# Performance work log

Measured on AMD Instinct MI355X. Metric: run time of the kernel, lower is better.

The kernel has to match this reference:

```python
import jax, jax.numpy as jnp
import numpy as np

N = 4096
D = 256
DEG = 32
E0 = N * DEG
RATIO = 0.5
NEG_SLOPE = 0.2


def setup_inputs() -> dict:
    key = jax.random.key(0)
    ks = jax.random.split(key, 12)
    # edges with NO self loops (so appending all N self-loops == add_remaining_self_loops)
    src = jax.random.randint(ks[0], (E0,), 0, N, dtype=jnp.int32)
    off = jax.random.randint(ks[1], (E0,), 1, N, dtype=jnp.int32)
    dst = ((src + off) % N).astype(jnp.int32)
    edge_index = jnp.stack([src, dst])
    edge_weight = jnp.ones((E0,), jnp.float32)
    x = jax.random.normal(ks[2], (N, D), jnp.float32)
    s = 1.0 / np.sqrt(D)
    u = lambda k, shp: jax.random.uniform(k, shp, jnp.float32, -s, s)
    return {
        'x': x,
        'edge_index': edge_index,
        'edge_weight': edge_weight,
        'lin_w': u(ks[3], (D, D)), 'lin_b': u(ks[4], (D,)),
        'att_w': jax.random.uniform(ks[5], (2 * D, 1), jnp.float32, -1.0 / np.sqrt(2 * D), 1.0 / np.sqrt(2 * D)),
        'att_b': u(ks[6], (1,)),
        'le1_w': u(ks[7], (D, 1)), 'le1_b': u(ks[8], (1,)),
        'le2_w': u(ks[9], (D, 1)),
        'le3_w': u(ks[10], (D, 1)), 'le3_b': u(ks[11], (1,)),
    }


def reference(x, edge_index, edge_weight, lin_w, lin_b, att_w, att_b,
              le1_w, le1_b, le2_w, le3_w, le3_b):
    n, d = x.shape
    # add_remaining_self_loops (input has no self loops by construction)
    loop = jnp.arange(n, dtype=edge_index.dtype)
    src = jnp.concatenate([edge_index[0], loop])
    dst = jnp.concatenate([edge_index[1], loop])
    w = jnp.concatenate([edge_weight, jnp.ones((n,), edge_weight.dtype)])

    # GNN is None -> x_pool = x
    x_pool_j = x[src]                                        # [E, D] gather
    x_q = jax.ops.segment_max(x_pool_j, dst, num_segments=n)  # scatter-max
    x_q_e = (x_q @ lin_w + lin_b)[dst]                        # [E, D]
    # att(cat([x_q, x_pool_j])) without materializing [E, 2D]
    score = x_q_e @ att_w[:d, 0] + x_pool_j @ att_w[d:, 0] + att_b[0]
    score = jax.nn.leaky_relu(score, NEG_SLOPE)
    # segment softmax over destination nodes
    smax = jax.ops.segment_max(score, dst, num_segments=n)
    ex = jnp.exp(score - smax[dst])
    denom = jax.ops.segment_sum(ex, dst, num_segments=n)
    score = ex / denom[dst]
    # dropout p=0 -> no-op
    xn = jax.ops.segment_sum(x_pool_j * score[:, None], dst, num_segments=n)

    # LEConv fitness: sigmoid( lin3(x) + sum_j (lin1(x_j) - lin2(x_i)) )
    a = xn @ le1_w + le1_b          # [N, 1]
    b = xn @ le2_w                  # [N, 1] (no bias)
    agg = jax.ops.segment_sum(a[src] - b[dst], dst, num_segments=n)
    fitness = jax.nn.sigmoid((agg + xn @ le3_w + le3_b)[:, 0])

    k = int(np.ceil(RATIO * N))
    _, perm = jax.lax.top_k(fitness, k)
    x_out = xn[perm] * fitness[perm][:, None]

    # Coarsening A_c = S[:, perm]^T @ A @ S[:, perm]; dense since SpGEMM nnz is data-dependent
    S = jnp.zeros((n, n), x.dtype).at[src, dst].add(score)[:, perm]  # [N, k]
    A = jnp.zeros((n, n), x.dtype).at[src, dst].add(w)               # [N, N]
    A_c = S.T @ (A @ S)                                              # [k, k]
    A_c = A_c * (1.0 - jnp.eye(k, dtype=A_c.dtype))                  # remove_diag
    return x_out, A_c, perm
```

## Files before the change

kernel.cpp:

```cpp
#include <hip/hip_runtime.h>
#include <cstdint>
#include <cstddef>
#include <math.h>

#define NN   4096
#define DD   256
#define E0S  131072
#define NE   (E0S + NN)
#define KK   2048
#define NEG_SLOPE 0.2f
#define SEGCAP 256

typedef float floatx4 __attribute__((ext_vector_type(4)));

__device__ __forceinline__ int esrc(const int* s, int e){ return e < E0S ? s[e] : e - E0S; }
__device__ __forceinline__ int edst(const int* d, int e){ return e < E0S ? d[e] : e - E0S; }

__global__ void init_kernel(int* deg_dst, int* deg_src, int* colmap, float* Ac, int zero_ac){
    int i = blockIdx.x * blockDim.x + threadIdx.x;
    int stride = gridDim.x * blockDim.x;
    if (zero_ac){
        for (size_t t = i; t < (size_t)KK * KK; t += stride) Ac[t] = 0.f;
    }
    for (int t = i; t < NN; t += stride){ deg_dst[t] = 0; deg_src[t] = 0; colmap[t] = -1; }
}

__global__ void count_kernel(const int* e_src, const int* e_dst, int* deg_dst, int* deg_src){
    int e = blockIdx.x * blockDim.x + threadIdx.x;
    if (e < NE){
        atomicAdd(&deg_dst[edst(e_dst, e)], 1);
        atomicAdd(&deg_src[esrc(e_src, e)], 1);
    }
}

__global__ void __launch_bounds__(1024) scan_kernel(const int* degA, int* offA, int* curA,
                                                    const int* degB, int* offB, int* curB){
    const int* deg = (blockIdx.x == 0) ? degA : degB;
    int* off = (blockIdx.x == 0) ? offA : offB;
    int* cur = (blockIdx.x == 0) ? curA : curB;
    __shared__ int part[1024];
    int t = threadIdx.x;
    int base = t * 4;
    int s0 = deg[base], s1 = deg[base+1], s2 = deg[base+2], s3 = deg[base+3];
    int tot = s0 + s1 + s2 + s3;
    part[t] = tot;
    __syncthreads();
    for (int d = 1; d < 1024; d <<= 1){
        int v = (t >= d) ? part[t - d] : 0;
        __syncthreads();
        part[t] += v;
        __syncthreads();
    }
    int excl = part[t] - tot;
    off[base]   = excl;            cur[base]   = excl;
    off[base+1] = excl + s0;       cur[base+1] = excl + s0;
    off[base+2] = excl + s0 + s1;  cur[base+2] = excl + s0 + s1;
    off[base+3] = excl + s0 + s1 + s2; cur[base+3] = excl + s0 + s1 + s2;
    if (t == 1023) off[NN] = part[1023];
}

__global__ void fill_kernel(const int* e_src, const int* e_dst, int* cur_dst, int* cur_src,
                            int* eid_dst, int* eid_src){
    int e = blockIdx.x * blockDim.x + threadIdx.x;
    if (e < NE){
        int p = atomicAdd(&cur_dst[edst(e_dst, e)], 1); eid_dst[p] = e;
        int q = atomicAdd(&cur_src[esrc(e_src, e)], 1); eid_src[q] = e;
    }
}

__global__ void segsort_kernel(const int* off_dst, int* eid_dst, const int* off_src, int* eid_src,
                               const int* e_src, int* isd){
    __shared__ int buf[4][SEGCAP];
    int wid  = (blockIdx.x * blockDim.x + threadIdx.x) >> 6;
    int lane = threadIdx.x & 63;
    int w    = threadIdx.x >> 6;
    const int* off; int* eid; int n; bool isdst;
    if (wid < NN){ off = off_dst; eid = eid_dst; n = wid; isdst = true; }
    else         { off = off_src; eid = eid_src; n = wid - NN; isdst = false; }
    int lo = off[n], hi = off[n+1];
    int L = hi - lo;
    int Lc = (L <= SEGCAP) ? L : SEGCAP;
    for (int i = lane; i < Lc; i += 64) buf[w][i] = eid[lo + i];
    __syncthreads();
    if (L <= SEGCAP){
        for (int i = lane; i < L; i += 64){
            int v = buf[w][i];
            int r = 0;
            for (int j = 0; j < L; ++j) r += (buf[w][j] < v);
            eid[lo + r] = v;
            if (isdst) isd[lo + r] = esrc(e_src, v);
        }
    } else if (lane == 0){
        for (int i = lo + 1; i < hi; ++i){
            int v = eid[i]; int j = i - 1;
            while (j >= lo && eid[j] > v){ eid[j+1] = eid[j]; --j; }
            eid[j+1] = v;
        }
        if (isdst) for (int i = lo; i < hi; ++i) isd[i] = esrc(e_src, eid[i]);
    }
}

__global__ void segmax_kernel(const float* x, const int* off, const int* isd, float* x_q){
    __shared__ int is_[4][SEGCAP];
    int g = threadIdx.x >> 6;
    int l = threadIdx.x & 63;
    int n = blockIdx.x * 4 + g;
    int lo = off[n], hi = off[n+1];
    int L = hi - lo;
    int Ls = (L <= SEGCAP) ? L : SEGCAP;
    for (int t = l; t < Ls; t += 64) is_[g][t] = isd[lo + t];
    __syncthreads();
    int c0 = l * 4;
    floatx4 m = {-INFINITY, -INFINITY, -INFINITY, -INFINITY};
    int t = 0;
    for (; t + 1 < Ls; t += 2){
        floatx4 v0 = *(const floatx4*)&x[(size_t)is_[g][t]   * DD + c0];
        floatx4 v1 = *(const floatx4*)&x[(size_t)is_[g][t+1] * DD + c0];
        m.x = fmaxf(m.x, fmaxf(v0.x, v1.x));
        m.y = fmaxf(m.y, fmaxf(v0.y, v1.y));
        m.z = fmaxf(m.z, fmaxf(v0.z, v1.z));
        m.w = fmaxf(m.w, fmaxf(v0.w, v1.w));
    }
    if (t < Ls){
        floatx4 v0 = *(const floatx4*)&x[(size_t)is_[g][t] * DD + c0];
        m.x = fmaxf(m.x, v0.x); m.y = fmaxf(m.y, v0.y);
        m.z = fmaxf(m.z, v0.z); m.w = fmaxf(m.w, v0.w);
    }
    for (t = Ls; t < L; ++t){
        floatx4 v0 = *(const floatx4*)&x[(size_t)isd[lo + t] * DD + c0];
        m.x = fmaxf(m.x, v0.x); m.y = fmaxf(m.y, v0.y);
        m.z = fmaxf(m.z, v0.z); m.w = fmaxf(m.w, v0.w);
    }
    *(floatx4*)&x_q[(size_t)n * DD + c0] = m;
}

#define LR2 4
__global__ void linnd_kernel(const float* x, const float* x_q,
                             const float* lin_w, const float* lin_b, const float* att_w,
                             float* q_s, float* p_s){
    __shared__ float xs[LR2][DD];
    __shared__ float s1[256], s2[256];
    int col = threadIdx.x;
    int r0 = blockIdx.x * LR2;
    for (int r = 0; r < LR2; ++r) xs[r][col] = x_q[(size_t)(r0 + r) * DD + col];
    __syncthreads();
    float acc[LR2];
    float bc = lin_b[col];
    #pragma unroll
    for (int r = 0; r < LR2; ++r) acc[r] = bc;
    for (int kk = 0; kk < DD; ++kk){
        float wv = lin_w[(size_t)kk * DD + col];
        #pragma unroll
        for (int r = 0; r < LR2; ++r) acc[r] = fmaf(xs[r][kk], wv, acc[r]);
    }
    float aw1 = att_w[col];
    float aw2 = att_w[DD + col];
    for (int r = 0; r < LR2; ++r){
        int n = r0 + r;
        s1[col] = acc[r] * aw1;
        s2[col] = x[(size_t)n * DD + col] * aw2;
        __syncthreads();
        for (int d = 128; d > 0; d >>= 1){
            if (col < d){ s1[col] += s1[col + d]; s2[col] += s2[col + d]; }
            __syncthreads();
        }
        if (col == 0){ q_s[n] = s1[0]; p_s[n] = s2[0]; }
        __syncthreads();
    }
}

__global__ void softxn_kernel(const float* x, const int* off, const int* eid, const int* isd,
                              const float* q_s, const float* p_s, const float* att_b,
                              const float* le1_w, const float* le1_b, const float* le2_w,
                              const float* le3_w, const float* le3_b,
                              float* sc, float* ssd, float* xn,
                              float* a_, float* b_, float* c_){
    __shared__ int   is_[SEGCAP];
    __shared__ float ss_[SEGCAP];
    __shared__ float s1[256], s2[256], s3[256];
    int n = blockIdx.x, col = threadIdx.x;
    int lo = off[n], hi = off[n+1];
    int L = hi - lo;
    int Ls = (L <= SEGCAP) ? L : SEGCAP;
    for (int t = col; t < Ls; t += 256) is_[t] = isd[lo + t];
    __syncthreads();
    if (col < 64){
        int lane = col;
        float ab = att_b[0];
        float qn = q_s[n];
        float m = -INFINITY;
        for (int t = lane; t < L; t += 64){
            int sn = (t < Ls) ? is_[t] : isd[lo + t];
            float s = qn + p_s[sn] + ab;
            s = (s > 0.f) ? s : NEG_SLOPE * s;
            m = fmaxf(m, s);
        }
        #pragma unroll
        for (int d = 32; d > 0; d >>= 1) m = fmaxf(m, __shfl_xor(m, d));
        float sum = 0.f;
        for (int t = lane; t < L; t += 64){
            int sn = (t < Ls) ? is_[t] : isd[lo + t];
            float s = qn + p_s[sn] + ab;
            s = (s > 0.f) ? s : NEG_SLOPE * s;
            float ex = expf(s - m);
            if (t < Ls) ss_[t] = ex; else ssd[lo + t] = ex;
            sum += ex;
        }
        #pragma unroll
        for (int d = 32; d > 0; d >>= 1) sum += __shfl_xor(sum, d);
        float inv = 1.f / sum;
        for (int t = lane; t < L; t += 64){
            float v = ((t < Ls) ? ss_[t] : ssd[lo + t]) * inv;
            if (t < Ls) ss_[t] = v;
            ssd[lo + t] = v;
            sc[eid[lo + t]] = v;
        }
    }
    __syncthreads();
    float acc = 0.f;
    int t = 0;
    for (; t + 1 < Ls; t += 2){
        float v0 = x[(size_t)is_[t]   * DD + col];
        float v1 = x[(size_t)is_[t+1] * DD + col];
        acc = fmaf(ss_[t],   v0, acc);
        acc = fmaf(ss_[t+1], v1, acc);
    }
    if (t < Ls) acc = fmaf(ss_[t], x[(size_t)is_[t] * DD + col], acc);
    for (t = Ls; t < L; ++t)
        acc = fmaf(ssd[lo + t], x[(size_t)isd[lo + t] * DD + col], acc);
    xn[(size_t)n * DD + col] = acc;
    s1[col] = acc * le1_w[col];
    s2[col] = acc * le2_w[col];
    s3[col] = acc * le3_w[col];
    __syncthreads();
    for (int dd = 128; dd > 0; dd >>= 1){
        if (col < dd){ s1[col] += s1[col+dd]; s2[col] += s2[col+dd]; s3[col] += s3[col+dd]; }
        __syncthreads();
    }
    if (col == 0){
        a_[n] = s1[0] + le1_b[0];
        b_[n] = s2[0];
        c_[n] = s3[0] + le3_b[0];
    }
}

__global__ void fitness_kernel(const int* off, const int* isd,
                               const float* a_, const float* b_, const float* c_,
                               float* fit){
    int wave = threadIdx.x >> 6;
    int lane = threadIdx.x & 63;
    int n = blockIdx.x * 4 + wave;
    int lo = off[n], hi = off[n+1];
    float bn = b_[n];
    float s = 0.f;
    for (int t = lo + lane; t < hi; t += 64){
        s += a_[isd[t]] - bn;
    }
    #pragma unroll
    for (int d = 32; d > 0; d >>= 1) s += __shfl_xor(s, d);
    if (lane == 0){
        float z = s + c_[n];
        fit[n] = 1.f / (1.f + expf(-z));
    }
}

__global__ void __launch_bounds__(1024) topk_kernel(const float* fit, int* perm, int* colmap,
                                                    float* out_perm){
    __shared__ unsigned long long keys[NN];
    int t = threadIdx.x;
    for (int i = t; i < NN; i += 1024){
        unsigned int u = __float_as_uint(fit[i]);
        u = (u & 0x80000000u) ? ~u : (u | 0x80000000u);
        u = ~u;
        keys[i] = ((unsigned long long)u << 32) | (unsigned int)i;
    }
    __syncthreads();
    for (unsigned int ssize = 2; ssize <= NN; ssize <<= 1){
        for (unsigned int stride = ssize >> 1; stride > 0; stride >>= 1){
            for (int i = t; i < NN / 2; i += 1024){
                unsigned int idx = 2u * i - (i & (stride - 1u));
                unsigned int par = idx + stride;
                bool asc = ((idx & ssize) == 0u);
                unsigned long long a = keys[idx], b = keys[par];
                if ((a > b) == asc){ keys[idx] = b; keys[par] = a; }
            }
            __syncthreads();
        }
    }
    for (int i = t; i < KK; i += 1024){
        int node = (int)(keys[i] & 0xFFFFFFFFull);
        perm[i] = node;
        colmap[node] = i;
        out_perm[i] = (float)node;
    }
}

__global__ void xoutprep_kernel(const float* xn, const float* fit, const int* perm, float* x_out,
                                const int* eid_src, const int* e_dst, const int* colmap,
                                const float* sc, int* cp, float* sp){
    int b = blockIdx.x;
    if (b < KK){
        int r = b, d = threadIdx.x;
        int p = perm[r];
        x_out[(size_t)r * DD + d] = xn[(size_t)p * DD + d] * fit[p];
    } else {
        int u = (b - KK) * 256 + threadIdx.x;
        if (u < NE){
            int f = eid_src[u];
            cp[u] = colmap[edst(e_dst, f)];
            sp[u] = sc[f];
        }
    }
}

__global__ void spgemm1_kernel(const int* e_dst, const float* ew,
                               const int* off_src, const int* eid_src,
                               const int* cp, const float* sp, float* T){
    __shared__ float row[KK];
    __shared__ int   jlo_[SEGCAP];
    __shared__ int   jhi_[SEGCAP];
    __shared__ float w_[SEGCAP];
    int i = blockIdx.x;
    for (int c = threadIdx.x; c < KK; c += 256) row[c] = 0.f;
    int lo = off_src[i], hi = off_src[i+1];
    int L = hi - lo;
    int Ls = (L <= SEGCAP) ? L : SEGCAP;
    for (int t = threadIdx.x; t < Ls; t += 256){
        int e = eid_src[lo + t];
        int j = edst(e_dst, e);
        jlo_[t] = off_src[j];
        jhi_[t] = off_src[j+1];
        w_[t]   = (e < E0S) ? ew[e] : 1.0f;
    }
    __syncthreads();
    int sw = threadIdx.x >> 5, ln = threadIdx.x & 31;
    for (int t = sw; t < Ls; t += 8){
        float w1 = w_[t];
        for (int u = jlo_[t] + ln; u < jhi_[t]; u += 32){
            int c = cp[u];
            if (c >= 0) atomicAdd(&row[c], w1 * sp[u]);
        }
    }
    for (int t = Ls + sw; t < L; t += 8){
        int e = eid_src[lo + t];
        int j = edst(e_dst, e);
        float w1 = (e < E0S) ? ew[e] : 1.0f;
        int jlo = off_src[j], jhi = off_src[j+1];
        for (int u = jlo + ln; u < jhi; u += 32){
            int c = cp[u];
            if (c >= 0) atomicAdd(&row[c], w1 * sp[u]);
        }
    }
    __syncthreads();
    float* Trow = T + (size_t)i * KK;
    for (int c = threadIdx.x; c < KK; c += 256) Trow[c] = row[c];
}

__global__ void spgemm2_kernel(const int* perm, const int* off_dst,
                               const int* isd, const float* ssd,
                               const float* T, float* Ac){
    __shared__ int   is_[8][SEGCAP];
    __shared__ float ss_[8][SEGCAP];
    int bx = blockIdx.x;
    int by = blockIdx.y;
    int half = by >> 8;
    int rr   = by & 255;
    int sub  = threadIdx.x >> 5;
    int lane = threadIdx.x & 31;
    int r = rr * 8 + sub;
    int chunk = bx + 8 * half;
    int c0 = chunk * 128 + lane * 4;
    int node = perm[r];
    int lo = off_dst[node], hi = off_dst[node+1];
    int L = hi - lo;
    int Ls = (L <= SEGCAP) ? L : SEGCAP;
    for (int t = lane; t < Ls; t += 32){
        is_[sub][t] = isd[lo + t];
        ss_[sub][t] = ssd[lo + t];
    }
    __syncthreads();
    floatx4 acc = {0.f, 0.f, 0.f, 0.f};
    int t = 0;
    for (; t + 1 < Ls; t += 2){
        floatx4 a = *(const floatx4*)&T[(size_t)is_[sub][t]   * KK + c0];
        floatx4 b = *(const floatx4*)&T[(size_t)is_[sub][t+1] * KK + c0];
        float s0 = ss_[sub][t], s1 = ss_[sub][t+1];
        acc.x = fmaf(s0, a.x, acc.x); acc.y = fmaf(s0, a.y, acc.y);
        acc.z = fmaf(s0, a.z, acc.z); acc.w = fmaf(s0, a.w, acc.w);
        acc.x = fmaf(s1, b.x, acc.x); acc.y = fmaf(s1, b.y, acc.y);
        acc.z = fmaf(s1, b.z, acc.z); acc.w = fmaf(s1, b.w, acc.w);
    }
    for (; t < Ls; ++t){
        floatx4 a = *(const floatx4*)&T[(size_t)is_[sub][t] * KK + c0];
        float s0 = ss_[sub][t];
        acc.x = fmaf(s0, a.x, acc.x); acc.y = fmaf(s0, a.y, acc.y);
        acc.z = fmaf(s0, a.z, acc.z); acc.w = fmaf(s0, a.w, acc.w);
    }
    for (t = Ls; t < L; ++t){
        floatx4 a = *(const floatx4*)&T[(size_t)isd[lo + t] * KK + c0];
        float s0 = ssd[lo + t];
        acc.x = fmaf(s0, a.x, acc.x); acc.y = fmaf(s0, a.y, acc.y);
        acc.z = fmaf(s0, a.z, acc.z); acc.w = fmaf(s0, a.w, acc.w);
    }
    if (r - c0 >= 0 && r - c0 < 4){
        if (r - c0 == 0) acc.x = 0.f;
        else if (r - c0 == 1) acc.y = 0.f;
        else if (r - c0 == 2) acc.z = 0.f;
        else acc.w = 0.f;
    }
    __builtin_nontemporal_store(acc, (floatx4*)&Ac[(size_t)r * KK + c0]);
}

__global__ void ac_kernel(const int* e_src, const int* e_dst, const float* ew,
                          const int* off_src,
                          const int* cp, const float* sp, float* Ac){
    int e1 = blockIdx.x * blockDim.x + threadIdx.x;
    if (e1 >= NE) return;
    int i = (e1 < E0S) ? e_src[e1] : e1 - E0S;
    int j = (e1 < E0S) ? e_dst[e1] : e1 - E0S;
    float w1 = (e1 < E0S) ? ew[e1] : 1.0f;
    int ilo = off_src[i], ihi = off_src[i+1];
    int jlo = off_src[j], jhi = off_src[j+1];
    for (int ta = ilo; ta < ihi; ++ta){
        int ca = cp[ta];
        if (ca < 0) continue;
        float va = sp[ta] * w1;
        float* rowp = Ac + (size_t)ca * KK;
        for (int tb = jlo; tb < jhi; ++tb){
            int cb = cp[tb];
            if (cb < 0) continue;
            atomicAdd(&rowp[cb], va * sp[tb]);
        }
    }
}

__global__ void diag_kernel(float* Ac){
    int r = blockIdx.x * blockDim.x + threadIdx.x;
    if (r < KK) Ac[(size_t)r * KK + r] = 0.f;
}

extern "C" void kernel_launch(void* const* d_in, const int* in_sizes, int n_in,
                              void* d_out, int out_size, void* d_ws, size_t ws_size,
                              hipStream_t stream){
    const float* x     = (const float*)d_in[0];
    const int*   ei    = (const int*)d_in[1];
    const float* ew    = (const float*)d_in[2];
    const float* lin_w = (const float*)d_in[3];
    const float* lin_b = (const float*)d_in[4];
    const float* att_w = (const float*)d_in[5];
    const float* att_b = (const float*)d_in[6];
    const float* le1_w = (const float*)d_in[7];
    const float* le1_b = (const float*)d_in[8];
    const float* le2_w = (const float*)d_in[9];
    const float* le3_w = (const float*)d_in[10];
    const float* le3_b = (const float*)d_in[11];

    const int* e_src = ei;
    const int* e_dst = ei + E0S;

    float* out    = (float*)d_out;
    float* x_out  = out;
    float* Ac     = out + (size_t)KK * DD;
    float* operm  = out + (size_t)KK * DD + (size_t)KK * KK;

    char* wp = (char*)d_ws;
    auto alloc_i = [&](size_t n){ int* p = (int*)wp; wp += n * sizeof(int); return p; };
    auto alloc_f = [&](size_t n){ float* p = (float*)wp; wp += n * sizeof(float); return p; };

    int* deg_dst = alloc_i(NN);
    int* deg_src = alloc_i(NN);
    int* off_dst = alloc_i(NN + 1);
    int* off_src = alloc_i(NN + 1);
    int* cur_dst = alloc_i(NN);
    int* cur_src = alloc_i(NN);
    int* eid_dst = alloc_i(NE);
    int* eid_src = alloc_i(NE);
    int* colmap  = alloc_i(NN);
    int* perm    = alloc_i(KK);
    int* isd     = alloc_i(NE);
    int* cp      = alloc_i(NE);
    float* sp    = alloc_f(NE);
    float* ssd   = alloc_f(NE);
    float* q_s   = alloc_f(NN);
    float* p_s   = alloc_f(NN);
    float* a_    = alloc_f(NN);
    float* b_    = alloc_f(NN);
    float* c_    = alloc_f(NN);
    float* fit   = alloc_f(NN);
    float* sc    = alloc_f(NE);
    float* x_q   = alloc_f((size_t)NN * DD);
    float* xn    = alloc_f((size_t)NN * DD);
    float* T     = alloc_f((size_t)NN * KK);
    bool dense_ok = ((size_t)(wp - (char*)d_ws) <= ws_size);
    (void)n_in; (void)in_sizes; (void)out_size;

    const int EB = (NE + 255) / 256;

    init_kernel<<<2048, 256, 0, stream>>>(deg_dst, deg_src, colmap, Ac, dense_ok ? 0 : 1);
    count_kernel<<<EB, 256, 0, stream>>>(e_src, e_dst, deg_dst, deg_src);
    scan_kernel<<<2, 1024, 0, stream>>>(deg_dst, off_dst, cur_dst, deg_src, off_src, cur_src);
    fill_kernel<<<EB, 256, 0, stream>>>(e_src, e_dst, cur_dst, cur_src, eid_dst, eid_src);
    segsort_kernel<<<(2 * NN) / 4, 256, 0, stream>>>(off_dst, eid_dst, off_src, eid_src, e_src, isd);
    segmax_kernel<<<NN / 4, 256, 0, stream>>>(x, off_dst, isd, x_q);
    linnd_kernel<<<NN / LR2, 256, 0, stream>>>(x, x_q, lin_w, lin_b, att_w, q_s, p_s);
    softxn_kernel<<<NN, 256, 0, stream>>>(x, off_dst, eid_dst, isd, q_s, p_s, att_b,
                                          le1_w, le1_b, le2_w, le3_w, le3_b,
                                          sc, ssd, xn, a_, b_, c_);
    fitness_kernel<<<NN / 4, 256, 0, stream>>>(off_dst, isd, a_, b_, c_, fit);
    topk_kernel<<<1, 1024, 0, stream>>>(fit, perm, colmap, operm);
    xoutprep_kernel<<<KK + EB, 256, 0, stream>>>(xn, fit, perm, x_out,
                                                 eid_src, e_dst, colmap, sc, cp, sp);
    if (dense_ok){
        spgemm1_kernel<<<NN, 256, 0, stream>>>(e_dst, ew, off_src, eid_src, cp, sp, T);
        spgemm2_kernel<<<dim3(8, 512), 256, 0, stream>>>(perm, off_dst, isd, ssd, T, Ac);
    } else {
        ac_kernel<<<EB, 256, 0, stream>>>(e_src, e_dst, ew, off_src, cp, sp, Ac);
        diag_kernel<<<(KK + 255) / 256, 256, 0, stream>>>(Ac);
    }
}
```

Before: 212.7 us.

## Process four nodes per block in softxn with float4 gathers and wave reductions

The softmax/aggregation kernel now assigns one 64-lane wave per destination node, with four nodes per block, instead of one 256-thread block per node. Each lane gathers four contiguous features with float4 loads, and the LEConv dot products use wave shuffles instead of a shared-memory tree reduction with repeated block barriers. Previously three of four waves sat idle during the softmax phase, and the reduction needed many __syncthreads; now every wave does useful work throughout. The init kernel also launches far fewer blocks when the Ac zeroing is not needed.

Result: faster. 204.5 us (-3.8%).

```diff
diff --git a/kernel.cpp b/kernel.cpp
--- a/kernel.cpp
+++ b/kernel.cpp
@@ -175,22 +175,22 @@
                               const float* le3_w, const float* le3_b,
                               float* sc, float* ssd, float* xn,
                               float* a_, float* b_, float* c_){
-    __shared__ int   is_[SEGCAP];
-    __shared__ float ss_[SEGCAP];
-    __shared__ float s1[256], s2[256], s3[256];
-    int n = blockIdx.x, col = threadIdx.x;
+    __shared__ int   is_[4][SEGCAP];
+    __shared__ float ss_[4][SEGCAP];
+    int g = threadIdx.x >> 6;
+    int l = threadIdx.x & 63;
+    int n = blockIdx.x * 4 + g;
     int lo = off[n], hi = off[n+1];
     int L = hi - lo;
     int Ls = (L <= SEGCAP) ? L : SEGCAP;
-    for (int t = col; t < Ls; t += 256) is_[t] = isd[lo + t];
-    __syncthreads();
-    if (col < 64){
-        int lane = col;
+    for (int t = l; t < Ls; t += 64) is_[g][t] = isd[lo + t];
+    __syncthreads();
+    {
         float ab = att_b[0];
         float qn = q_s[n];
         float m = -INFINITY;
-        for (int t = lane; t < L; t += 64){
-            int sn = (t < Ls) ? is_[t] : isd[lo + t];
+        for (int t = l; t < L; t += 64){
+            int sn = (t < Ls) ? is_[g][t] : isd[lo + t];
             float s = qn + p_s[sn] + ab;
             s = (s > 0.f) ? s : NEG_SLOPE * s;
             m = fmaxf(m, s);
@@ -198,49 +198,72 @@
         #pragma unroll
         for (int d = 32; d > 0; d >>= 1) m = fmaxf(m, __shfl_xor(m, d));
         float sum = 0.f;
-        for (int t = lane; t < L; t += 64){
-            int sn = (t < Ls) ? is_[t] : isd[lo + t];
+        for (int t = l; t < L; t += 64){
+            int sn = (t < Ls) ? is_[g][t] : isd[lo + t];
             float s = qn + p_s[sn] + ab;
             s = (s > 0.f) ? s : NEG_SLOPE * s;
             float ex = expf(s - m);
-            if (t < Ls) ss_[t] = ex; else ssd[lo + t] = ex;
+            if (t < Ls) ss_[g][t] = ex; else ssd[lo + t] = ex;
             sum += ex;
         }
         #pragma unroll
         for (int d = 32; d > 0; d >>= 1) sum += __shfl_xor(sum, d);
         float inv = 1.f / sum;
-        for (int t = lane; t < L; t += 64){
-            float v = ((t < Ls) ? ss_[t] : ssd[lo + t]) * inv;
-            if (t < Ls) ss_[t] = v;
+        for (int t = l; t < L; t += 64){
+            float v = ((t < Ls) ? ss_[g][t] : ssd[lo + t]) * inv;
+            if (t < Ls) ss_[g][t] = v;
             ssd[lo + t] = v;
             sc[eid[lo + t]] = v;
         }
     }
     __syncthreads();
-    float acc = 0.f;
+    int c0 = l * 4;
+    floatx4 acc = {0.f, 0.f, 0.f, 0.f};
     int t = 0;
     for (; t + 1 < Ls; t += 2){
-        float v0 = x[(size_t)is_[t]   * DD + col];
-        float v1 = x[(size_t)is_[t+1] * DD + col];
-        acc = fmaf(ss_[t],   v0, acc);
-        acc = fmaf(ss_[t+1], v1, acc);
-    }
-    if (t < Ls) acc = fmaf(ss_[t], x[(size_t)is_[t] * DD + col], acc);
-    for (t = Ls; t < L; ++t)
-        acc = fmaf(ssd[lo + t], x[(size_t)isd[lo + t] * DD + col], acc);
-    xn[(size_t)n * DD + col] = acc;
-    s1[col] = acc * le1_w[col];
-    s2[col] = acc * le2_w[col];
-    s3[col] = acc * le3_w[col];
-    __syncthreads();
-    for (int dd = 128; dd > 0; dd >>= 1){
-        if (col < dd){ s1[col] += s1[col+dd]; s2[col] += s2[col+dd]; s3[col] += s3[col+dd]; }
-        __syncthreads();
-    }
-    if (col == 0){
-        a_[n] = s1[0] + le1_b[0];
-        b_[n] = s2[0];
-        c_[n] = s3[0] + le3_b[0];
+        floatx4 v0 = *(const floatx4*)&x[(size_t)is_[g][t]   * DD + c0];
+        floatx4 v1 = *(const floatx4*)&x[(size_t)is_[g][t+1] * DD + c0];
+        float s0 = ss_[g][t], s1 = ss_[g][t+1];
+        acc.x = fmaf(s0, v0.x, acc.x); acc.y = fmaf(s0, v0.y, acc.y);
+        acc.z = fmaf(s0, v0.z, acc.z); acc.w = fmaf(s0, v0.w, acc.w);
+        acc.x = fmaf(s1, v1.x, acc.x); acc.y = fmaf(s1, v1.y, acc.y);
+        acc.z = fmaf(s1, v1.z, acc.z); acc.w = fmaf(s1, v1.w, acc.w);
+    }
+    if (t < Ls){
+        floatx4 v0 = *(const floatx4*)&x[(size_t)is_[g][t] * DD + c0];
+        float s0 = ss_[g][t];
+        acc.x = fmaf(s0, v0.x, acc.x); acc.y = fmaf(s0, v0.y, acc.y);
+        acc.z = fmaf(s0, v0.z, acc.z); acc.w = fmaf(s0, v0.w, acc.w);
+    }
+    for (t = Ls; t < L; ++t){
+        floatx4 v0 = *(const floatx4*)&x[(size_t)isd[lo + t] * DD + c0];
+        float s0 = ssd[lo + t];
+        acc.x = fmaf(s0, v0.x, acc.x); acc.y = fmaf(s0, v0.y, acc.y);
+        acc.z = fmaf(s0, v0.z, acc.z); acc.w = fmaf(s0, v0.w, acc.w);
+    }
+    *(floatx4*)&xn[(size_t)n * DD + c0] = acc;
+    floatx4 w1 = *(const floatx4*)&le1_w[c0];
+    floatx4 w2 = *(const floatx4*)&le2_w[c0];
+    floatx4 w3 = *(const floatx4*)&le3_w[c0];
+    floatx4 v1 = acc * w1;
+    floatx4 v2 = acc * w2;
+    floatx4 v3 = acc * w3;
+    #pragma unroll
+    for (int m = 32; m >= 1; m >>= 1){
+        v1.x += __shfl_xor(v1.x, m); v1.y += __shfl_xor(v1.y, m);
+        v1.z += __shfl_xor(v1.z, m); v1.w += __shfl_xor(v1.w, m);
+        v2.x += __shfl_xor(v2.x, m); v2.y += __shfl_xor(v2.y, m);
+        v2.z += __shfl_xor(v2.z, m); v2.w += __shfl_xor(v2.w, m);
+        v3.x += __shfl_xor(v3.x, m); v3.y += __shfl_xor(v3.y, m);
+        v3.z += __shfl_xor(v3.z, m); v3.w += __shfl_xor(v3.w, m);
+    }
+    if (l == 0){
+        v1.x += v1.z; v1.y += v1.w; v1.x += v1.y;
+        v2.x += v2.z; v2.y += v2.w; v2.x += v2.y;
+        v3.x += v3.z; v3.y += v3.w; v3.x += v3.y;
+        a_[n] = v1.x + le1_b[0];
+        b_[n] = v2.x;
+        c_[n] = v3.x + le3_b[0];
     }
 }
 
@@ -496,16 +519,17 @@
 
     const int EB = (NE + 255) / 256;
 
-    init_kernel<<<2048, 256, 0, stream>>>(deg_dst, deg_src, colmap, Ac, dense_ok ? 0 : 1);
+    init_kernel<<<dense_ok ? 64 : 2048, 256, 0, stream>>>(deg_dst, deg_src, colmap, Ac,
+                                                          dense_ok ? 0 : 1);
     count_kernel<<<EB, 256, 0, stream>>>(e_src, e_dst, deg_dst, deg_src);
     scan_kernel<<<2, 1024, 0, stream>>>(deg_dst, off_dst, cur_dst, deg_src, off_src, cur_src);
     fill_kernel<<<EB, 256, 0, stream>>>(e_src, e_dst, cur_dst, cur_src, eid_dst, eid_src);
     segsort_kernel<<<(2 * NN) / 4, 256, 0, stream>>>(off_dst, eid_dst, off_src, eid_src, e_src, isd);
     segmax_kernel<<<NN / 4, 256, 0, stream>>>(x, off_dst, isd, x_q);
     linnd_kernel<<<NN / LR2, 256, 0, stream>>>(x, x_q, lin_w, lin_b, att_w, q_s, p_s);
-    softxn_kernel<<<NN, 256, 0, stream>>>(x, off_dst, eid_dst, isd, q_s, p_s, att_b,
-                                          le1_w, le1_b, le2_w, le3_w, le3_b,
-                                          sc, ssd, xn, a_, b_, c_);
+    softxn_kernel<<<NN / 4, 256, 0, stream>>>(x, off_dst, eid_dst, isd, q_s, p_s, att_b,
+                                              le1_w, le1_b, le2_w, le3_w, le3_b,
+                                              sc, ssd, xn, a_, b_, c_);
     fitness_kernel<<<NN / 4, 256, 0, stream>>>(off_dst, isd, a_, b_, c_, fit);
     topk_kernel<<<1, 1024, 0, stream>>>(fit, perm, colmap, operm);
     xoutprep_kernel<<<KK + EB, 256, 0, stream>>>(xn, fit, perm, x_out,
```
